# Kernel tuning notes

Hardware: AMD Instinct MI355X
Metric: run time of the kernel (lower is better)

The kernel has to match this reference:

```python
import jax, jax.numpy as jnp
import numpy as np

TWO_PI = 2.0 * np.pi
EPS = 1e-6

# mixture packed layout along last axis (7): [weight, px, py, cxx, cxy, cyx, cyy]

def unpack(m):
    w = m[..., 0]
    p = m[..., 1:3]
    C = m[..., 3:7].reshape(m.shape[:-1] + (2, 2))
    return w, p, C

def pack(w, p, C):
    return jnp.concatenate([w[..., None], p, C.reshape(C.shape[:-2] + (4,))], axis=-1)

def det2(C):
    return C[..., 0, 0] * C[..., 1, 1] - C[..., 0, 1] * C[..., 1, 0]

def inv2(C):
    d = det2(C)[..., None, None]
    adj = jnp.stack([
        jnp.stack([C[..., 1, 1], -C[..., 0, 1]], axis=-1),
        jnp.stack([-C[..., 1, 0], C[..., 0, 0]], axis=-1)], axis=-2)
    return adj / d

def component_integrals(w, C):
    # integral of an amplitude-parameterized 2D gaussian: w * 2*pi * sqrt(det C)
    return w * TWO_PI * jnp.sqrt(jnp.maximum(det2(C), EPS))

def gm_convolve(data, kernel):
    # data [B,Li,Nd,7], kernel [Lo,Li,Nk,7] -> [B,Lo,Li*Nd*Nk,7]
    wd, pd, Cd = unpack(data)
    wk, pk, Ck = unpack(kernel)
    dd = det2(Cd)[:, None, :, :, None]              # [B,1,Li,Nd,1]
    dk = det2(Ck)[None, :, :, None, :]              # [1,Lo,Li,1,Nk]
    Cs = Cd[:, None, :, :, None, :, :] + Ck[None, :, :, None, :, :, :]  # [B,Lo,Li,Nd,Nk,2,2]
    ps = pd[:, None, :, :, None, :] + pk[None, :, :, None, :, :]        # [B,Lo,Li,Nd,Nk,2]
    # amplitude of convolved gaussian so that integrals multiply
    ws = (wd[:, None, :, :, None] * wk[None, :, :, None, :]
          * TWO_PI * jnp.sqrt(dd * dk / jnp.maximum(det2(Cs), EPS)))
    m = pack(ws, ps, Cs)
    B, Lo = m.shape[0], m.shape[1]
    return m.reshape(B, Lo, -1, 7)

def eval_at_centers(w, p, C):
    # value of the whole mixture at each component center; [.., N]
    Ci = inv2(C)                                        # [..,N,2,2]
    diff = p[..., :, None, :] - p[..., None, :, :]      # [..,K,N,2]
    md = jnp.einsum('...kni,...nij,...knj->...kn', diff, Ci, diff)
    return jnp.einsum('...n,...kn->...k', w, jnp.exp(-0.5 * md))

def relu_fit(m, bias, n_out):
    # fitting-based ReLU: rescale each component so the mixture matches
    # relu(m(x)+b) at the centers, then keep the n_out largest components
    w, p, C = unpack(m)
    v = eval_at_centers(w, p, C) + bias[None, :, None]  # [B,L,N]
    scale = jax.nn.relu(v) / (jnp.abs(v) + EPS)
    w2 = w * scale
    _, idx = jax.lax.top_k(jnp.abs(w2), n_out)          # [B,L,n_out]
    w_s = jnp.take_along_axis(w2, idx, axis=-1)
    p_s = jnp.take_along_axis(p, jnp.broadcast_to(idx[..., None], idx.shape + (2,)), axis=-2)
    Cf = C.reshape(C.shape[:-2] + (4,))
    C_s = jnp.take_along_axis(Cf, jnp.broadcast_to(idx[..., None], idx.shape + (4,)), axis=-2)
    return pack(w_s, p_s, C_s.reshape(C_s.shape[:-1] + (2, 2)))

def batchnorm(m, per_gaussian):
    w, p, C = unpack(m)
    tot = jnp.sum(jnp.abs(component_integrals(w, C)), axis=-1, keepdims=True)  # [B,L,1]
    if not per_gaussian:
        tot = jnp.mean(tot, axis=0, keepdims=True)      # batch statistic per channel
    return pack(w / (tot + EPS), p, C)

def integrate(m):
    w, _, C = unpack(m)
    return jnp.sum(component_integrals(w, C), axis=-1)  # [B,L]

def forward(in_x, kernel1, kernel2, kernel3, bias1, bias2, bias3):
    x = batchnorm(in_x, per_gaussian=True)   # bn0
    x = gm_convolve(x, kernel1)              # [B,5,320,7]
    x = relu_fit(x, bias1, 25)
    x = batchnorm(x, per_gaussian=False)
    x = gm_convolve(x, kernel2)              # [B,6,625,7]
    x = relu_fit(x, bias2, 12)
    x = batchnorm(x, per_gaussian=False)
    x = gm_convolve(x, kernel3)              # [B,10,360,7]
    x = relu_fit(x, bias3, 5)
    x = batchnorm(x, per_gaussian=False)
    out = jax.nn.log_softmax(integrate(x), axis=1)
    return out.reshape(-1, 10)

def _make_kernel(key, lo, li, nk, weight_sd, position_range, covariance_range):
    kw, kp = jax.random.split(key)
    w = jax.random.normal(kw, (lo, li, nk)) * weight_sd
    p = jax.random.uniform(kp, (lo, li, nk, 2), minval=-position_range, maxval=position_range)
    C = jnp.broadcast_to(covariance_range * jnp.eye(2), (lo, li, nk, 2, 2))
    return pack(w, p, C).astype(jnp.float32)

def setup_inputs() -> dict:
    key = jax.random.key(0)
    k = jax.random.split(key, 8)
    B, NIN, NK = 32, 64, 5
    w = jax.random.uniform(k[0], (B, 1, NIN), minval=0.05, maxval=1.0)
    p = jax.random.uniform(k[1], (B, 1, NIN, 2), minval=-14.0, maxval=14.0)
    cdiag = jax.random.uniform(k[2], (B, 1, NIN, 2), minval=0.5, maxval=2.0)
    C = jnp.zeros((B, 1, NIN, 2, 2)).at[..., 0, 0].set(cdiag[..., 0]).at[..., 1, 1].set(cdiag[..., 1])
    in_x = pack(w, p, C).astype(jnp.float32)
    return {
        'in_x': in_x,
        'kernel1': _make_kernel(k[3], 5, 1, NK, 0.4, 2.0, 0.5),
        'kernel2': _make_kernel(k[4], 6, 5, NK, 0.04, 4.0, 2.0),
        'kernel3': _make_kernel(k[5], 10, 6, NK, 0.025, 8.0, 4.0),
        'bias1': jnp.zeros((5,), jnp.float32),
        'bias2': jnp.zeros((6,), jnp.float32),
        'bias3': jnp.zeros((10,), jnp.float32),
    }

def reference(in_x, kernel1, kernel2, kernel3, bias1, bias2, bias3):
    return forward(in_x, kernel1, kernel2, kernel3, bias1, bias2, bias3)
```

## Files before the change

### kernel.cpp

```cpp
#include <hip/hip_runtime.h>

#define TWO_PI_F 6.283185307179586f
#define EPS_F 1e-6f
#define LOG2E_F 1.4426950408889634f
#define BATCH 32

#if __has_builtin(__builtin_amdgcn_exp2f)
#define EXP2F(x) __builtin_amdgcn_exp2f(x)
#else
#define EXP2F(x) exp2f(x)
#endif

typedef float v2f __attribute__((ext_vector_type(2)));

__device__ __forceinline__ float sane(float x) {
    return ((__float_as_uint(x) & 0x7f800000u) == 0x7f800000u) ? 0.f : x;
}

template<int LO, int LI, int ND, int NK, int NCOMP, int KOUT,
         int KP, int TPG, int G, bool FIRST>
__global__ __launch_bounds__(TPG*G) void layer_kernel(
    const float* __restrict__ in_x,
    const float* __restrict__ prev_sel,
    const float* __restrict__ prev_tot,
    const float* __restrict__ kern,
    const float* __restrict__ bias,
    float* __restrict__ out_sel,
    float* __restrict__ out_tot)
{
    constexpr int KUSE   = NCOMP / KP;
    static_assert(KUSE * KP == NCOMP, "exact k tiling required");
    constexpr int NT     = TPG * G;
    constexpr int CHUNK  = (NCOMP + G - 1) / G;
    constexpr int NPADT  = G*CHUNK + 4;
    constexpr int NCOMP4 = (NCOMP + 3) & ~3;
    constexpr int NQn    = NCOMP4 / 4;
    constexpr int NPAIR  = KP / 2;
    constexpr int PPAD   = NPAIR > 0 ? NPAIR : 1;
    constexpr bool ODD   = (KP & 1) != 0;

    const int b   = blockIdx.x / LO;
    const int lo  = blockIdx.x % LO;
    const int tid = threadIdx.x;
    const int g   = tid / TPG;
    const int kt  = tid % TPG;
    const bool active = (kt < KUSE);

    struct StageT {
        float4 d_c[LI*ND];
        float4 k_c[LI*NK];
        float  d_w[LI*ND], d_px[LI*ND], d_py[LI*ND];
        float  k_w[LI*NK], k_px[LI*NK], k_py[LI*NK];
    };
    constexpr size_t ACCB = (size_t)(G > 1 ? (G-1)*TPG*KP : 1) * sizeof(float);
    constexpr size_t UB   = sizeof(StageT) > ACCB ? sizeof(StageT) : ACCB;
    __shared__ __align__(16) unsigned char u_smem[UB];
    StageT& st    = *reinterpret_cast<StageT*>(u_smem);
    float* accbuf = reinterpret_cast<float*>(u_smem);

    __shared__ float2 cPos[NCOMP];
    __shared__ float4 nP[NPADT];
    __shared__ float4 nQ[NPADT];
    __shared__ float4 cC[NCOMP];
    __shared__ float  w2s[NCOMP];
    __shared__ __align__(16) float a2s[NCOMP4];
    __shared__ __align__(16) float scr[64];
    __shared__ float  selint[32];
    __shared__ float  dscale[LI];
    __shared__ float  ptot[FIRST ? 1 : BATCH*LI];

    if constexpr (FIRST) {
        if (tid < ND) {
            const float* s = in_x + (size_t)(b*ND + tid)*7;
            const float w  = sane(s[0]);
            const float c0 = sane(s[3]), c1 = sane(s[4]), c2 = sane(s[5]), c3 = sane(s[6]);
            st.d_w[tid] = w; st.d_px[tid] = sane(s[1]); st.d_py[tid] = sane(s[2]);
            st.d_c[tid] = make_float4(c0, c1, c2, c3);
            const float det = c0*c3 - c1*c2;
            scr[tid] = sane(fabsf(w) * TWO_PI_F * sqrtf(fmaxf(det, EPS_F)));
        }
        __syncthreads();
        if (tid == 0) {
            float s = 0.f;
            const float4* s4 = (const float4*)scr;
            for (int i = 0; i < 16; ++i) {
                const float4 v = s4[i];
                s += v.x; s += v.y; s += v.z; s += v.w;
            }
            dscale[0] = 1.f / (s + EPS_F);
        }
        __syncthreads();
        if (tid < ND) st.d_w[tid] = sane(st.d_w[tid] * dscale[0]);
    } else {
        for (int i = tid; i < BATCH*LI; i += NT) ptot[i] = prev_tot[i];
        __syncthreads();
        if (tid < LI) {
            float s = 0.f;
            #pragma unroll 1
            for (int bb = 0; bb < BATCH; ++bb) s += ptot[bb*LI + tid];
            dscale[tid] = 1.f / (s / (float)BATCH + EPS_F);
        }
        __syncthreads();
        if (tid < LI*ND) {
            const int li = tid / ND;
            const float* s = prev_sel + (size_t)(b*LI*ND + tid)*7;
            st.d_w[tid]  = sane(s[0] * dscale[li]);
            st.d_px[tid] = s[1]; st.d_py[tid] = s[2];
            st.d_c[tid]  = make_float4(s[3], s[4], s[5], s[6]);
        }
    }
    if (tid < LI*NK) {
        const float* s = kern + (size_t)(lo*LI*NK + tid)*7;
        st.k_w[tid]  = sane(s[0]);
        st.k_px[tid] = sane(s[1]); st.k_py[tid] = sane(s[2]);
        st.k_c[tid]  = make_float4(sane(s[3]), sane(s[4]), sane(s[5]), sane(s[6]));
    }
    __syncthreads();

    if (tid < NCOMP) {
        const int li = tid / (ND*NK);
        const int r  = tid % (ND*NK);
        const int nd = r / NK, nk = r % NK;
        const int di = li*ND + nd, ki = li*NK + nk;
        const float4 dc = st.d_c[di], kc = st.k_c[ki];
        const float c0 = dc.x + kc.x, c1 = dc.y + kc.y, c2 = dc.z + kc.z, c3 = dc.w + kc.w;
        const float dd = dc.x*dc.w - dc.y*dc.z;
        const float dk = kc.x*kc.w - kc.y*kc.z;
        const float ds = c0*c3 - c1*c2;
        const float w  = sane(st.d_w[di]*st.k_w[ki]*TWO_PI_F*sqrtf(fmaxf(dd*dk, 0.f) / fmaxf(ds, EPS_F)));
        const float px = sane(st.d_px[di] + st.k_px[ki]);
        const float py = sane(st.d_py[di] + st.k_py[ki]);
        const float inv = -0.5f * LOG2E_F / ds;
        const float a   = sane(c3*inv);
        const float bb  = sane(-(c1 + c2)*inv);
        const float cc  = sane(c0*inv);
        const float dd2 = sane(-(2.f*a*px + bb*py));
        const float ee  = sane(-(2.f*cc*py + bb*px));
        const float ff  = sane((a*px + bb*py)*px + cc*py*py);
        cPos[tid] = make_float2(px, py);
        nP[tid]   = make_float4(a, bb, cc, dd2);
        nQ[tid]   = make_float4(ee, ff, w, 0.f);
        cC[tid]   = make_float4(sane(c0), sane(c1), sane(c2), sane(c3));
    }
    for (int i = NCOMP + tid; i < NPADT; i += NT) {
        nP[i] = make_float4(0.f, 0.f, 0.f, 0.f);
        nQ[i] = make_float4(0.f, 0.f, 0.f, 0.f);
    }
    __syncthreads();

    v2f kxP[PPAD], kyP[PPAD], kx2P[PPAD], ky2P[PPAD], kxyP[PPAD], accP[PPAD];
    float kxS = 0.f, kyS = 0.f, kx2S = 0.f, ky2S = 0.f, kxyS = 0.f, accS = 0.f;
    #pragma unroll
    for (int p = 0; p < NPAIR; ++p) {
        float x0 = 0.f, y0 = 0.f, x1 = 0.f, y1 = 0.f;
        if (active) {
            const float2 p0 = cPos[kt + (2*p    )*KUSE];
            const float2 p1 = cPos[kt + (2*p + 1)*KUSE];
            x0 = p0.x; y0 = p0.y; x1 = p1.x; y1 = p1.y;
        }
        v2f kx; kx.x = x0; kx.y = x1;
        v2f ky; ky.x = y0; ky.y = y1;
        kxP[p] = kx; kyP[p] = ky;
        kx2P[p] = kx*kx; ky2P[p] = ky*ky; kxyP[p] = kx*ky;
        v2f z; z.x = 0.f; z.y = 0.f; accP[p] = z;
    }
    if constexpr (ODD) {
        if (active) { const float2 pz = cPos[kt + (KP-1)*KUSE]; kxS = pz.x; kyS = pz.y; }
        kx2S = kxS*kxS; ky2S = kyS*kyS; kxyS = kxS*kyS;
    }
    {
        const int n0 = g*CHUNK;
        const float4* __restrict__ bP = &nP[n0];
        const float4* __restrict__ bQ = &nQ[n0];
        float4 P0 = bP[0], Q0 = bQ[0];
        float4 P1 = bP[1], Q1 = bQ[1];
        float4 P2 = bP[2], Q2 = bQ[2];
        float4 P3 = bP[3], Q3 = bQ[3];
        int nr = 4;

#define PHB_STEP(PP,QQ)                                                       \
        {   const float4 Pn_ = bP[nr], Qn_ = bQ[nr]; ++nr;                    \
            v2f Pa; Pa.x = PP.x; Pa.y = PP.x;                                 \
            v2f Pb; Pb.x = PP.y; Pb.y = PP.y;                                 \
            v2f Pc; Pc.x = PP.z; Pc.y = PP.z;                                 \
            v2f Pd; Pd.x = PP.w; Pd.y = PP.w;                                 \
            v2f Qe; Qe.x = QQ.x; Qe.y = QQ.x;                                 \
            v2f Qf; Qf.x = QQ.y; Qf.y = QQ.y;                                 \
            v2f Qw; Qw.x = QQ.z; Qw.y = QQ.z;                                 \
            _Pragma("unroll")                                                 \
            for (int p = 0; p < NPAIR; ++p) {                                 \
                const v2f md = __builtin_elementwise_fma(Pa, kx2P[p],         \
                               __builtin_elementwise_fma(Pb, kxyP[p],         \
                               __builtin_elementwise_fma(Pc, ky2P[p],         \
                               __builtin_elementwise_fma(Pd, kxP[p],          \
                               __builtin_elementwise_fma(Qe, kyP[p], Qf)))));  \
                v2f ex; ex.x = EXP2F(md.x); ex.y = EXP2F(md.y);               \
                accP[p] = __builtin_elementwise_fma(Qw, ex, accP[p]);         \
            }                                                                 \
            if constexpr (ODD) {                                              \
                const float md = fmaf(PP.x, kx2S,                             \
                                 fmaf(PP.y, kxyS,                             \
                                 fmaf(PP.z, ky2S,                             \
                                 fmaf(PP.w, kxS,                              \
                                 fmaf(QQ.x, kyS, QQ.y)))));                   \
                accS = fmaf(QQ.z, EXP2F(md), accS);                           \
            }                                                                 \
            PP = Pn_; QQ = Qn_; }

        #pragma unroll 1
        for (int i4 = 0; i4 < CHUNK/4; ++i4) {
            PHB_STEP(P0, Q0)
            PHB_STEP(P1, Q1)
            PHB_STEP(P2, Q2)
            PHB_STEP(P3, Q3)
        }
        if constexpr ((CHUNK % 4) >= 1) PHB_STEP(P0, Q0)
        if constexpr ((CHUNK % 4) >= 2) PHB_STEP(P1, Q1)
        if constexpr ((CHUNK % 4) >= 3) PHB_STEP(P2, Q2)
#undef PHB_STEP
    }
    float acc[KP];
    #pragma unroll
    for (int p = 0; p < NPAIR; ++p) { acc[2*p] = accP[p].x; acc[2*p+1] = accP[p].y; }
    if constexpr (ODD) acc[KP-1] = accS;

    if (g > 0 && active) {
        #pragma unroll
        for (int j = 0; j < KP; ++j) accbuf[((g-1)*TPG + kt)*KP + j] = acc[j];
    }
    __syncthreads();

    const float bi = bias[lo];
    if (g == 0 && active) {
        #pragma unroll
        for (int j = 0; j < KP; ++j) {
            float s = acc[j];
            for (int gg = 1; gg < G; ++gg) s += accbuf[((gg-1)*TPG + kt)*KP + j];
            const float v  = s + bi;
            const float sc = fmaxf(v, 0.f) / (fabsf(v) + EPS_F);
            const int   k  = kt + j*KUSE;
            const float ww = sane(nQ[k].z * sc);
            w2s[k] = ww;
            a2s[k] = fabsf(ww);
        }
    }
    if constexpr (NCOMP4 > NCOMP) {
        if (tid >= NCOMP && tid < NCOMP4) a2s[tid] = -1.f;
    }
    __syncthreads();

    constexpr int CQ = (NQn + G - 1) / G;
    int rank[KP];
    float myv[KP];
    #pragma unroll
    for (int j = 0; j < KP; ++j) rank[j] = 0;
    if (active) {
        #pragma unroll
        for (int j = 0; j < KP; ++j) myv[j] = a2s[kt + j*KUSE];
        const int q0 = g*CQ;
        const int q1 = (q0 + CQ < NQn) ? (q0 + CQ) : NQn;
        for (int q = q0; q < q1; ++q) {
            const float4 v4 = ((const float4*)a2s)[q];
            #pragma unroll
            for (int c = 0; c < 4; ++c) {
                const float vj = (c == 0) ? v4.x : (c == 1) ? v4.y : (c == 2) ? v4.z : v4.w;
                const int   jj = 4*q + c;
                #pragma unroll
                for (int j = 0; j < KP; ++j) {
                    const int myk = kt + j*KUSE;
                    rank[j] += (vj > myv[j] || (vj == myv[j] && jj < myk)) ? 1 : 0;
                }
            }
        }
        if (g > 0) {
            #pragma unroll
            for (int j = 0; j < KP; ++j) accbuf[((g-1)*TPG + kt)*KP + j] = (float)rank[j];
        }
    }
    __syncthreads();

    if (g == 0 && active) {
        #pragma unroll
        for (int j = 0; j < KP; ++j) {
            int r = rank[j];
            for (int gg = 1; gg < G; ++gg) r += (int)accbuf[((gg-1)*TPG + kt)*KP + j];
            if (r < KOUT) {
                const int k = kt + j*KUSE;
                const float2 p = cPos[k];
                const float4 c = cC[k];
                const float ww = w2s[k];
                float* dst = out_sel + (size_t)((b*LO + lo)*KOUT + r)*7;
                dst[0] = ww; dst[1] = p.x; dst[2] = p.y;
                dst[3] = c.x; dst[4] = c.y; dst[5] = c.z; dst[6] = c.w;
                const float det = c.x*c.w - c.y*c.z;
                selint[r] = sane(fabsf(ww) * TWO_PI_F * sqrtf(fmaxf(det, EPS_F)));
            }
        }
    }
    __syncthreads();
    if (tid == 0) {
        float s = 0.f;
        for (int i = 0; i < KOUT; ++i) s += selint[i];
        out_tot[b*LO + lo] = s;
    }
}

__global__ __launch_bounds__(64) void final_kernel(
    const float* __restrict__ sel3,
    const float* __restrict__ tot3,
    float* __restrict__ out)
{
    const int b = blockIdx.x;
    const int tid = threadIdx.x;
    __shared__ float scale3[10], integ[10], red2[2];
    if (tid < 10) {
        float s = 0.f;
        for (int bb = 0; bb < BATCH; ++bb) s += tot3[bb*10 + tid];
        scale3[tid] = 1.f / (s / (float)BATCH + EPS_F);
    }
    __syncthreads();
    if (tid < 10) {
        float s = 0.f;
        const float* base = sel3 + (size_t)((b*10 + tid)*5)*7;
        for (int kk = 0; kk < 5; ++kk) {
            const float* c = base + kk*7;
            const float det = c[3]*c[6] - c[4]*c[5];
            s += c[0] * scale3[tid] * TWO_PI_F * sqrtf(fmaxf(det, EPS_F));
        }
        integ[tid] = sane(s);
    }
    __syncthreads();
    if (tid == 0) {
        float m = -1e30f;
        for (int l = 0; l < 10; ++l) m = fmaxf(m, integ[l]);
        float ss = 0.f;
        for (int l = 0; l < 10; ++l) ss += __expf(integ[l] - m);
        red2[0] = m; red2[1] = logf(ss);
    }
    __syncthreads();
    if (tid < 10) out[b*10 + tid] = integ[tid] - red2[0] - red2[1];
}

extern "C" void kernel_launch(void* const* d_in, const int* in_sizes, int n_in,
                              void* d_out, int out_size, void* d_ws, size_t ws_size,
                              hipStream_t stream)
{
    const float* in_x = (const float*)d_in[0];
    const float* k1   = (const float*)d_in[1];
    const float* k2   = (const float*)d_in[2];
    const float* k3   = (const float*)d_in[3];
    const float* b1   = (const float*)d_in[4];
    const float* b2   = (const float*)d_in[5];
    const float* b3   = (const float*)d_in[6];
    float* out = (float*)d_out;

    float* ws = (float*)d_ws;
    float* sel1 = ws;
    float* tot1 = ws + 28000;
    float* sel2 = ws + 28160;
    float* tot2 = ws + 44288;
    float* sel3 = ws + 44480;
    float* tot3 = ws + 55680;

    layer_kernel<5, 1, 64, 5, 320, 25, 5, 64, 16, true><<<BATCH*5, 1024, 0, stream>>>(
        in_x, nullptr, nullptr, k1, b1, sel1, tot1);
    layer_kernel<6, 5, 25, 5, 625, 12, 5, 128, 8, false><<<BATCH*6, 1024, 0, stream>>>(
        nullptr, sel1, tot1, k2, b2, sel2, tot2);
    layer_kernel<10, 6, 12, 5, 360, 5, 6, 64, 12, false><<<BATCH*10, 768, 0, stream>>>(
        nullptr, sel2, tot2, k3, b3, sel3, tot3);
    final_kernel<<<BATCH, 64, 0, stream>>>(sel3, tot3, out);
}
```

Before: 147.6 us.

## Split layer-2 evaluation across four blocks per unit with separate finalize kernel

Layer 2 used one 1024-thread block per (batch, output channel), which gave only 192 blocks. It is now split into a partial kernel that launches four 256-thread blocks per unit, each evaluating a quarter of the component groups and writing partial sums to global memory. A separate finalize kernel reduces the partials, applies the ReLU rescale and does the top-K rank selection. The aim is better occupancy across the GPU's compute units. The cost is an extra kernel launch, global round trips for the partials and component data, and redundant staging and component construction in every split block.

```diff
diff --git a/kernel.cpp b/kernel.cpp
--- a/kernel.cpp
+++ b/kernel.cpp
@@ -305,6 +305,282 @@
     }
 }
 
+template<int LO, int LI, int ND, int NK, int NCOMP,
+         int KP, int TPG, int G, int NSPLIT, bool FIRST>
+__global__ __launch_bounds__(TPG*(G/NSPLIT)) void layer_partial(
+    const float* __restrict__ in_x,
+    const float* __restrict__ prev_sel,
+    const float* __restrict__ prev_tot,
+    const float* __restrict__ kern,
+    float* __restrict__ comp7,
+    float* __restrict__ gpart)
+{
+    constexpr int KUSE  = NCOMP / KP;
+    static_assert(KUSE * KP == NCOMP, "exact k tiling required");
+    static_assert(G % NSPLIT == 0, "split along group boundaries");
+    constexpr int GBLK  = G / NSPLIT;
+    constexpr int NT    = TPG * GBLK;
+    constexpr int CHUNK = (NCOMP + G - 1) / G;
+    constexpr int NPADT = G*CHUNK + 4;
+    constexpr int GSTR  = (NCOMP + 7) & ~7;
+    constexpr int NPAIR = KP / 2;
+    constexpr int PPAD  = NPAIR > 0 ? NPAIR : 1;
+    constexpr bool ODD  = (KP & 1) != 0;
+    static_assert(NT >= LI*ND && NT >= LI*NK && NT >= LI, "one-pass staging");
+
+    const int s    = blockIdx.x % NSPLIT;
+    const int unit = blockIdx.x / NSPLIT;
+    const int lo   = unit % LO;
+    const int b    = unit / LO;
+    const int tid  = threadIdx.x;
+    const int gl   = tid / TPG;
+    const int gg   = s*GBLK + gl;
+    const int kt   = tid % TPG;
+    const bool active = (kt < KUSE);
+
+    __shared__ struct {
+        float4 d_c[LI*ND];
+        float4 k_c[LI*NK];
+        float  d_w[LI*ND], d_px[LI*ND], d_py[LI*ND];
+        float  k_w[LI*NK], k_px[LI*NK], k_py[LI*NK];
+    } st;
+    __shared__ float2 cPos[NCOMP];
+    __shared__ float4 nP[NPADT];
+    __shared__ float4 nQ[NPADT];
+    __shared__ __align__(16) float scr[64];
+    __shared__ float dscale[LI];
+    __shared__ float ptot[FIRST ? 1 : BATCH*LI];
+
+    if constexpr (FIRST) {
+        if (tid < ND) {
+            const float* sp = in_x + (size_t)(b*ND + tid)*7;
+            const float w  = sane(sp[0]);
+            const float c0 = sane(sp[3]), c1 = sane(sp[4]), c2 = sane(sp[5]), c3 = sane(sp[6]);
+            st.d_w[tid] = w; st.d_px[tid] = sane(sp[1]); st.d_py[tid] = sane(sp[2]);
+            st.d_c[tid] = make_float4(c0, c1, c2, c3);
+            const float det = c0*c3 - c1*c2;
+            scr[tid] = sane(fabsf(w) * TWO_PI_F * sqrtf(fmaxf(det, EPS_F)));
+        }
+        __syncthreads();
+        if (tid == 0) {
+            float ssum = 0.f;
+            const float4* s4 = (const float4*)scr;
+            for (int i = 0; i < 16; ++i) {
+                const float4 v = s4[i];
+                ssum += v.x; ssum += v.y; ssum += v.z; ssum += v.w;
+            }
+            dscale[0] = 1.f / (ssum + EPS_F);
+        }
+        __syncthreads();
+        if (tid < ND) st.d_w[tid] = sane(st.d_w[tid] * dscale[0]);
+    } else {
+        for (int i = tid; i < BATCH*LI; i += NT) ptot[i] = prev_tot[i];
+        __syncthreads();
+        if (tid < LI) {
+            float ssum = 0.f;
+            #pragma unroll 1
+            for (int bb = 0; bb < BATCH; ++bb) ssum += ptot[bb*LI + tid];
+            dscale[tid] = 1.f / (ssum / (float)BATCH + EPS_F);
+        }
+        __syncthreads();
+        if (tid < LI*ND) {
+            const int li = tid / ND;
+            const float* sp = prev_sel + (size_t)(b*LI*ND + tid)*7;
+            st.d_w[tid]  = sane(sp[0] * dscale[li]);
+            st.d_px[tid] = sp[1]; st.d_py[tid] = sp[2];
+            st.d_c[tid]  = make_float4(sp[3], sp[4], sp[5], sp[6]);
+        }
+    }
+    if (tid < LI*NK) {
+        const float* sp = kern + (size_t)(lo*LI*NK + tid)*7;
+        st.k_w[tid]  = sane(sp[0]);
+        st.k_px[tid] = sane(sp[1]); st.k_py[tid] = sane(sp[2]);
+        st.k_c[tid]  = make_float4(sane(sp[3]), sane(sp[4]), sane(sp[5]), sane(sp[6]));
+    }
+    __syncthreads();
+
+    for (int i = tid; i < NCOMP; i += NT) {
+        const int li = i / (ND*NK);
+        const int rr = i % (ND*NK);
+        const int nd = rr / NK, nk = rr % NK;
+        const int di = li*ND + nd, ki = li*NK + nk;
+        const float4 dc = st.d_c[di], kc = st.k_c[ki];
+        const float c0 = dc.x + kc.x, c1 = dc.y + kc.y, c2 = dc.z + kc.z, c3 = dc.w + kc.w;
+        const float dd = dc.x*dc.w - dc.y*dc.z;
+        const float dk = kc.x*kc.w - kc.y*kc.z;
+        const float ds = c0*c3 - c1*c2;
+        const float w  = sane(st.d_w[di]*st.k_w[ki]*TWO_PI_F*sqrtf(fmaxf(dd*dk, 0.f) / fmaxf(ds, EPS_F)));
+        const float px = sane(st.d_px[di] + st.k_px[ki]);
+        const float py = sane(st.d_py[di] + st.k_py[ki]);
+        const float inv = -0.5f * LOG2E_F / ds;
+        const float a   = sane(c3*inv);
+        const float bb  = sane(-(c1 + c2)*inv);
+        const float cc  = sane(c0*inv);
+        const float dd2 = sane(-(2.f*a*px + bb*py));
+        const float ee  = sane(-(2.f*cc*py + bb*px));
+        const float ff  = sane((a*px + bb*py)*px + cc*py*py);
+        cPos[i] = make_float2(px, py);
+        nP[i]   = make_float4(a, bb, cc, dd2);
+        nQ[i]   = make_float4(ee, ff, w, 0.f);
+        if (s == 0) {
+            float* c7 = comp7 + ((size_t)unit*NCOMP + i)*8;
+            *(float4*)c7       = make_float4(w, px, py, sane(c0));
+            *(float4*)(c7 + 4) = make_float4(sane(c1), sane(c2), sane(c3), 0.f);
+        }
+    }
+    for (int i = NCOMP + tid; i < NPADT; i += NT) {
+        nP[i] = make_float4(0.f, 0.f, 0.f, 0.f);
+        nQ[i] = make_float4(0.f, 0.f, 0.f, 0.f);
+    }
+    __syncthreads();
+
+    v2f kxP[PPAD], kyP[PPAD], kx2P[PPAD], ky2P[PPAD], kxyP[PPAD], accP[PPAD];
+    float kxS = 0.f, kyS = 0.f, kx2S = 0.f, ky2S = 0.f, kxyS = 0.f, accS = 0.f;
+    #pragma unroll
+    for (int p = 0; p < NPAIR; ++p) {
+        float x0 = 0.f, y0 = 0.f, x1 = 0.f, y1 = 0.f;
+        if (active) {
+            const float2 p0 = cPos[kt + (2*p    )*KUSE];
+            const float2 p1 = cPos[kt + (2*p + 1)*KUSE];
+            x0 = p0.x; y0 = p0.y; x1 = p1.x; y1 = p1.y;
+        }
+        v2f kx; kx.x = x0; kx.y = x1;
+        v2f ky; ky.x = y0; ky.y = y1;
+        kxP[p] = kx; kyP[p] = ky;
+        kx2P[p] = kx*kx; ky2P[p] = ky*ky; kxyP[p] = kx*ky;
+        v2f z; z.x = 0.f; z.y = 0.f; accP[p] = z;
+    }
+    if constexpr (ODD) {
+        if (active) { const float2 pz = cPos[kt + (KP-1)*KUSE]; kxS = pz.x; kyS = pz.y; }
+        kx2S = kxS*kxS; ky2S = kyS*kyS; kxyS = kxS*kyS;
+    }
+    {
+        const int n0 = gg*CHUNK;
+        const float4* __restrict__ bP = &nP[n0];
+        const float4* __restrict__ bQ = &nQ[n0];
+        float4 P0 = bP[0], Q0 = bQ[0];
+        float4 P1 = bP[1], Q1 = bQ[1];
+        float4 P2 = bP[2], Q2 = bQ[2];
+        float4 P3 = bP[3], Q3 = bQ[3];
+        int nr = 4;
+
+#define PHB_STEP(PP,QQ)                                                       \
+        {   const float4 Pn_ = bP[nr], Qn_ = bQ[nr]; ++nr;                    \
+            v2f Pa; Pa.x = PP.x; Pa.y = PP.x;                                 \
+            v2f Pb; Pb.x = PP.y; Pb.y = PP.y;                                 \
+            v2f Pc; Pc.x = PP.z; Pc.y = PP.z;                                 \
+            v2f Pd; Pd.x = PP.w; Pd.y = PP.w;                                 \
+            v2f Qe; Qe.x = QQ.x; Qe.y = QQ.x;                                 \
+            v2f Qf; Qf.x = QQ.y; Qf.y = QQ.y;                                 \
+            v2f Qw; Qw.x = QQ.z; Qw.y = QQ.z;                                 \
+            _Pragma("unroll")                                                 \
+            for (int p = 0; p < NPAIR; ++p) {                                 \
+                const v2f md = __builtin_elementwise_fma(Pa, kx2P[p],         \
+                               __builtin_elementwise_fma(Pb, kxyP[p],         \
+                               __builtin_elementwise_fma(Pc, ky2P[p],         \
+                               __builtin_elementwise_fma(Pd, kxP[p],          \
+                               __builtin_elementwise_fma(Qe, kyP[p], Qf)))));  \
+                v2f ex; ex.x = EXP2F(md.x); ex.y = EXP2F(md.y);               \
+                accP[p] = __builtin_elementwise_fma(Qw, ex, accP[p]);         \
+            }                                                                 \
+            if constexpr (ODD) {                                              \
+                const float md = fmaf(PP.x, kx2S,                             \
+                                 fmaf(PP.y, kxyS,                             \
+                                 fmaf(PP.z, ky2S,                             \
+                                 fmaf(PP.w, kxS,                              \
+                                 fmaf(QQ.x, kyS, QQ.y)))));                   \
+                accS = fmaf(QQ.z, EXP2F(md), accS);                           \
+            }                                                                 \
+            PP = Pn_; QQ = Qn_; }
+
+        #pragma unroll 1
+        for (int i4 = 0; i4 < CHUNK/4; ++i4) {
+            PHB_STEP(P0, Q0)
+            PHB_STEP(P1, Q1)
+            PHB_STEP(P2, Q2)
+            PHB_STEP(P3, Q3)
+        }
+        if constexpr ((CHUNK % 4) >= 1) PHB_STEP(P0, Q0)
+        if constexpr ((CHUNK % 4) >= 2) PHB_STEP(P1, Q1)
+        if constexpr ((CHUNK % 4) >= 3) PHB_STEP(P2, Q2)
+#undef PHB_STEP
+    }
+    float acc[KP];
+    #pragma unroll
+    for (int p = 0; p < NPAIR; ++p) { acc[2*p] = accP[p].x; acc[2*p+1] = accP[p].y; }
+    if constexpr (ODD) acc[KP-1] = accS;
+
+    if (active) {
+        float* gp = gpart + ((size_t)unit*G + gg)*GSTR;
+        #pragma unroll
+        for (int j = 0; j < KP; ++j) gp[kt + j*KUSE] = acc[j];
+    }
+}
+
+template<int LO, int NCOMP, int KOUT, int G, int NTC>
+__global__ __launch_bounds__(NTC) void layer_finalize(
+    const float* __restrict__ comp7,
+    const float* __restrict__ gpart,
+    const float* __restrict__ bias,
+    float* __restrict__ out_sel,
+    float* __restrict__ out_tot)
+{
+    constexpr int GSTR   = (NCOMP + 7) & ~7;
+    constexpr int NCOMP4 = (NCOMP + 3) & ~3;
+    constexpr int NQn    = NCOMP4 / 4;
+    const int unit = blockIdx.x;
+    const int lo   = unit % LO;
+    const int tid  = threadIdx.x;
+
+    __shared__ float w2s[NCOMP];
+    __shared__ __align__(16) float a2s[NCOMP4];
+    __shared__ float selint[32];
+
+    const float bi = bias[lo];
+    const float* gb = gpart + (size_t)unit*G*GSTR;
+    for (int k = tid; k < NCOMP; k += NTC) {
+        float ssum = gb[k];
+        #pragma unroll 1
+        for (int gg = 1; gg < G; ++gg) ssum += gb[(size_t)gg*GSTR + k];
+        const float v  = ssum + bi;
+        const float sc = fmaxf(v, 0.f) / (fabsf(v) + EPS_F);
+        const float ww = sane(comp7[((size_t)unit*NCOMP + k)*8] * sc);
+        w2s[k] = ww;
+        a2s[k] = fabsf(ww);
+    }
+    for (int i = NCOMP + tid; i < NCOMP4; i += NTC) a2s[i] = -1.f;
+    __syncthreads();
+
+    for (int k = tid; k < NCOMP; k += NTC) {
+        const float mv = a2s[k];
+        int r = 0;
+        for (int q = 0; q < NQn; ++q) {
+            const float4 v4 = ((const float4*)a2s)[q];
+            const int j4 = 4*q;
+            r += (v4.x > mv || (v4.x == mv && j4     < k)) ? 1 : 0;
+            r += (v4.y > mv || (v4.y == mv && j4 + 1 < k)) ? 1 : 0;
+            r += (v4.z > mv || (v4.z == mv && j4 + 2 < k)) ? 1 : 0;
+            r += (v4.w > mv || (v4.w == mv && j4 + 3 < k)) ? 1 : 0;
+        }
+        if (r < KOUT) {
+            const float4 c0 = *(const float4*)&comp7[((size_t)unit*NCOMP + k)*8];
+            const float4 c1 = *(const float4*)&comp7[((size_t)unit*NCOMP + k)*8 + 4];
+            const float ww = w2s[k];
+            float* dst = out_sel + (size_t)(unit*KOUT + r)*7;
+            dst[0] = ww; dst[1] = c0.y; dst[2] = c0.z;
+            dst[3] = c0.w; dst[4] = c1.x; dst[5] = c1.y; dst[6] = c1.z;
+            const float det = c0.w*c1.z - c1.x*c1.y;
+            selint[r] = sane(fabsf(ww) * TWO_PI_F * sqrtf(fmaxf(det, EPS_F)));
+        }
+    }
+    __syncthreads();
+    if (tid == 0) {
+        float ssum = 0.f;
+        for (int i = 0; i < KOUT; ++i) ssum += selint[i];
+        out_tot[unit] = ssum;
+    }
+}
+
 __global__ __launch_bounds__(64) void final_kernel(
     const float* __restrict__ sel3,
     const float* __restrict__ tot3,
@@ -361,11 +637,15 @@
     float* tot2 = ws + 44288;
     float* sel3 = ws + 44480;
     float* tot3 = ws + 55680;
+    float* comp7_2 = ws + 56000;
+    float* gpart2  = ws + 1016000;
 
     layer_kernel<5, 1, 64, 5, 320, 25, 5, 64, 16, true><<<BATCH*5, 1024, 0, stream>>>(
         in_x, nullptr, nullptr, k1, b1, sel1, tot1);
-    layer_kernel<6, 5, 25, 5, 625, 12, 5, 128, 8, false><<<BATCH*6, 1024, 0, stream>>>(
-        nullptr, sel1, tot1, k2, b2, sel2, tot2);
+    layer_partial<6, 5, 25, 5, 625, 5, 128, 8, 4, false>
+        <<<BATCH*6*4, 256, 0, stream>>>(nullptr, sel1, tot1, k2, comp7_2, gpart2);
+    layer_finalize<6, 625, 12, 8, 640><<<BATCH*6, 640, 0, stream>>>(
+        comp7_2, gpart2, b2, sel2, tot2);
     layer_kernel<10, 6, 12, 5, 360, 5, 6, 64, 12, false><<<BATCH*10, 768, 0, stream>>>(
         nullptr, sel2, tot2, k3, b3, sel3, tot3);
     final_kernel<<<BATCH, 64, 0, stream>>>(sel3, tot3, out);
```

Measured after the change: 156.2 us. 5.8% more time.
